# Kernel tuning notes

Hardware: AMD Instinct MI355X
Metric: run time of the kernel (lower is better)

## Reference

```python
import jax, jax.numpy as jnp
import numpy as np

N, D, F, K = 50000, 256, 256, 10


def setup_inputs() -> dict:
    key = jax.random.key(0)
    k1, k2, k3, k4, k5, k6 = jax.random.split(key, 6)
    # neighbor indices in [-1, N); -1 marks padding (masked out in forward)
    return {
        "Z1": jax.random.normal(k1, (N, D), dtype=jnp.float32),
        "Z2": jax.random.normal(k2, (N, D), dtype=jnp.float32),
        "Wr": jax.random.normal(k3, (D, F), dtype=jnp.float32),
        "Wnr": jax.random.normal(k4, (D, F), dtype=jnp.float32),
        "n1": jax.random.randint(k5, (N, K), -1, N, dtype=jnp.int64),
        "n2": jax.random.randint(k6, (N, K), -1, N, dtype=jnp.int64),
    }


def _protein(Z, nb, Wr, Wnr):
    residues_signal = Z @ Wr                      # [N, F]
    neighbors_base_signal = Z @ Wnr               # [N, F]
    mask = (nb > -1)                              # [N, K]
    # index -1 wraps to last row (as in torch), then is zeroed by the mask
    feats = neighbors_base_signal[nb] * mask[..., None].astype(Z.dtype)  # [N, K, F]
    norm = jnp.maximum(mask.sum(axis=1), 1).astype(Z.dtype)[:, None]     # [N, 1]
    neighbors_signal = feats.sum(axis=1) / norm
    return jax.nn.relu(residues_signal + neighbors_signal)


def reference(Z1, Z2, Wr, Wnr, n1, n2):
    out1 = _protein(Z1, n1, Wr, Wnr)
    out2 = _protein(Z2, n2, Wr, Wnr)
    return jnp.stack([out1, out2])  # [2, N, F]
```

## Files before the change

kernel.cpp:

```cpp
#include <hip/hip_runtime.h>
#include <hip/hip_bf16.h>
#include <hip/hip_fp8.h>

#define NNODE 50000
#define MTOT  100000
#define NF    256
#define KNB   10

typedef unsigned short u16;
typedef float f32x4 __attribute__((ext_vector_type(4)));
typedef float f32x2 __attribute__((ext_vector_type(2)));
typedef short bf16x8 __attribute__((ext_vector_type(8)));

__device__ __forceinline__ u16 f2bf(float f) {
    unsigned u = __builtin_bit_cast(unsigned, f);
    unsigned r = (u + 0x7fffu + ((u >> 16) & 1u)) >> 16;
    return (u16)r;
}
__device__ __forceinline__ unsigned char f2f8(float f) {
    return (unsigned char)__hip_fp8_e4m3(f).__x;
}
__device__ __forceinline__ float f8tof(unsigned char b) {
    __hip_fp8_e4m3 h;
    h.__x = (__hip_fp8_storage_t)b;
    return (float)h;
}
template <int WORD>
__device__ __forceinline__ f32x2 cvt2_fp8(unsigned v) {
#if __has_builtin(__builtin_amdgcn_cvt_pk_f32_fp8)
    auto c = __builtin_amdgcn_cvt_pk_f32_fp8((int)v, WORD);
    f32x2 r; r.x = c[0]; r.y = c[1];
    return r;
#else
    unsigned s = WORD ? (v >> 16) : v;
    f32x2 r;
    r.x = f8tof((unsigned char)(s & 0xff));
    r.y = f8tof((unsigned char)((s >> 8) & 0xff));
    return r;
#endif
}
template <int WORD>
__device__ __forceinline__ unsigned pk_fp8(float a, float b, unsigned old) {
#if __has_builtin(__builtin_amdgcn_cvt_pk_fp8_f32)
    return (unsigned)__builtin_amdgcn_cvt_pk_fp8_f32(a, b, (int)old, WORD);
#else
    unsigned lo = (unsigned)f2f8(a) | ((unsigned)f2f8(b) << 8);
    return WORD ? ((old & 0x0000ffffu) | (lo << 16)) : ((old & 0xffff0000u) | lo);
#endif
}
__device__ __forceinline__ void gload_lds16(const void* g, void* l) {
    __builtin_amdgcn_global_load_lds(
        (const __attribute__((address_space(1))) unsigned int*)g,
        (__attribute__((address_space(3))) unsigned int*)l, 16, 0, 0);
}

__global__ __launch_bounds__(256) void cast_all(const float* __restrict__ Z1,
                                                const float* __restrict__ Z2,
                                                const float* __restrict__ Wr,
                                                const float* __restrict__ Wnr,
                                                u16* __restrict__ Zleft,
                                                unsigned char* __restrict__ Z8,
                                                u16* __restrict__ WT,
                                                unsigned char* __restrict__ WT8) {
    int b = blockIdx.x;
    if (b < 12500) {
        unsigned id = b * 256 + threadIdx.x;
        int m = id >> 5;
        int d = (id & 31) << 3;
        const float* src = (m < NNODE) ? (Z1 + (size_t)m * 256 + d)
                                       : (Z2 + (size_t)(m - NNODE) * 256 + d);
        float4 a = *(const float4*)src;
        float4 bb = *(const float4*)(src + 4);
        uint4 o;
        o.x = (unsigned)f2bf(a.x) | ((unsigned)f2bf(a.y) << 16);
        o.y = (unsigned)f2bf(a.z) | ((unsigned)f2bf(a.w) << 16);
        o.z = (unsigned)f2bf(bb.x) | ((unsigned)f2bf(bb.y) << 16);
        o.w = (unsigned)f2bf(bb.z) | ((unsigned)f2bf(bb.w) << 16);
        *(uint4*)(Zleft + (size_t)m * 256 + d) = o;
        uint2 o8;
        o8.x = (unsigned)f2f8(a.x) | ((unsigned)f2f8(a.y) << 8) |
               ((unsigned)f2f8(a.z) << 16) | ((unsigned)f2f8(a.w) << 24);
        o8.y = (unsigned)f2f8(bb.x) | ((unsigned)f2f8(bb.y) << 8) |
               ((unsigned)f2f8(bb.z) << 16) | ((unsigned)f2f8(bb.w) << 24);
        *(uint2*)(Z8 + (size_t)m * 256 + d) = o8;
    } else if (b < 12756) {
        int id = (b - 12500) * 256 + threadIdx.x;
        int n = id >> 8, k = id & 255;
        WT[n * 256 + k] = f2bf(Wr[(size_t)k * 256 + n]);
    } else {
        int id = (b - 12756) * 256 + threadIdx.x;
        int n = id >> 8, k = id & 255;
        int kb = k ^ (((n >> 2) & 1) << 3);
        WT8[n * 256 + kb] = f2f8(Wnr[(size_t)k * 256 + n]);
    }
}

__device__ __forceinline__ void stageA(const u16* __restrict__ Zl, u16* dst,
                                       int m0, int kt, int t) {
    int row = t >> 3, gd = t & 7;
    int gs = gd ^ (row & 7);
    int grow = m0 + row;
    if (grow >= MTOT) grow = MTOT - 1;
    gload_lds16(Zl + (size_t)grow * 256 + kt + gs * 8, dst + t * 8);
}
__device__ __forceinline__ void stageBl(const u16* __restrict__ WT, u16* dst,
                                        int kt, int t) {
    #pragma unroll
    for (int rp = 0; rp < 4; ++rp) {
        int c = rp * 512 + t;
        int col = c >> 3, gd = c & 7;
        int gs = gd ^ (col & 7);
        gload_lds16(WT + (size_t)col * 256 + kt + gs * 8, dst + c * 8);
    }
}
__device__ __forceinline__ void stageBr(const unsigned char* __restrict__ WT8,
                                        unsigned char* dst, int ktr, int t) {
    #pragma unroll
    for (int rp = 0; rp < 2; ++rp) {
        int c = rp * 512 + t;
        int col = c >> 2, gd = c & 3;
        int gs = gd ^ (col & 3);
        gload_lds16(WT8 + (size_t)col * 256 + ktr + gs * 16, dst + c * 16);
    }
}

__device__ __forceinline__ void mfma_left(const u16* sAc, const u16* sBc, int lane,
                                          int wr, int wc, f32x4 (&acc)[2][4]) {
    const int hi = lane >> 4, l15 = lane & 15;
    #pragma unroll
    for (int kk = 0; kk < 64; kk += 32) {
        int g = (kk >> 3) + hi;
        bf16x8 af[2], bfr[4];
        #pragma unroll
        for (int i = 0; i < 2; ++i) {
            int row = wr * 32 + i * 16 + l15;
            af[i] = *(const bf16x8*)((const char*)sAc + row * 128 + ((g ^ (row & 7)) << 4));
        }
        #pragma unroll
        for (int j = 0; j < 4; ++j) {
            int col = wc * 64 + j * 16 + l15;
            bfr[j] = *(const bf16x8*)((const char*)sBc + col * 128 + ((g ^ (col & 7)) << 4));
        }
        #pragma unroll
        for (int i = 0; i < 2; ++i)
            #pragma unroll
            for (int j = 0; j < 4; ++j)
                acc[i][j] = __builtin_amdgcn_mfma_f32_16x16x32_bf16(af[i], bfr[j], acc[i][j], 0, 0, 0);
    }
}
__device__ __forceinline__ void mfma_right(const unsigned char* sZ, const unsigned char* sBc,
                                           int R, int lane, int wr, int wc,
                                           f32x4 (&acc)[2][4]) {
    const int hi = lane >> 4, l15 = lane & 15;
    #pragma unroll
    for (int m = 0; m < 2; ++m) {
        long long az[2], bz[4];
        #pragma unroll
        for (int i = 0; i < 2; ++i) {
            int row = wr * 32 + i * 16 + l15;
            int g8 = R * 8 + m * 4 + hi;
            az[i] = *(const long long*)(sZ + row * 256 + ((g8 ^ (row & 7)) << 3));
        }
        #pragma unroll
        for (int j = 0; j < 4; ++j) {
            int col = wc * 64 + j * 16 + l15;
            int G = 2 * m + (hi >> 1);
            int hb = ((hi & 1) ^ ((col >> 2) & 1)) << 3;
            bz[j] = *(const long long*)(sBc + col * 64 + ((G ^ (col & 3)) << 4) + hb);
        }
        #pragma unroll
        for (int i = 0; i < 2; ++i)
            #pragma unroll
            for (int j = 0; j < 4; ++j)
                acc[i][j] = __builtin_amdgcn_mfma_f32_16x16x32_fp8_fp8(az[i], bz[j], acc[i][j], 0, 0, 0);
    }
}

__device__ __forceinline__ void consume(const uint2 (&gv)[KNB], unsigned mask, int cnt,
                                        int w, int lane, int s, unsigned char* sZ) {
    f32x2 a0 = {0.f, 0.f}, a1 = {0.f, 0.f}, a2 = {0.f, 0.f}, a3 = {0.f, 0.f};
    #pragma unroll
    for (int k = 0; k < KNB; ++k) {
        float mm = (float)((mask >> k) & 1u);
        f32x2 m2 = {mm, mm};
        a0 += m2 * cvt2_fp8<0>(gv[k].x);
        a1 += m2 * cvt2_fp8<1>(gv[k].x);
        a2 += m2 * cvt2_fp8<0>(gv[k].y);
        a3 += m2 * cvt2_fp8<1>(gv[k].y);
    }
    float sc = 1.0f / (float)(cnt > 0 ? cnt : 1);
    unsigned w0 = pk_fp8<0>(a0.x * sc, a0.y * sc, 0u);
    w0 = pk_fp8<1>(a1.x * sc, a1.y * sc, w0);
    unsigned w1 = pk_fp8<0>(a2.x * sc, a2.y * sc, 0u);
    w1 = pk_fp8<1>(a3.x * sc, a3.y * sc, w1);
    int rl = w * 8 + s * 2 + (lane >> 5);
    int gp = (lane & 31) ^ (rl & 7);
    *(uint2*)(sZ + rl * 256 + (gp << 3)) = make_uint2(w0, w1);
}

template <int S>
__device__ __forceinline__ void left_step(const u16* __restrict__ Zl,
                                          const u16* __restrict__ WT,
                                          const unsigned char* __restrict__ Z8,
                                          const int* __restrict__ n1,
                                          const int* __restrict__ n2,
                                          u16* sA0, u16* sA1, u16* sBL, unsigned char* sZ,
                                          int m0, int t, int lane, int w, int wr, int wc,
                                          int2 (&icur)[5], unsigned& pmask, int& pcnt,
                                          uint2 (&gv)[KNB], f32x4 (&acc)[2][4]) {
    u16* sAcur = (S & 1) ? sA1 : sA0;
    u16* sAnxt = (S & 1) ? sA0 : sA1;
    stageBl(WT, sBL, S * 64, t);
    __builtin_amdgcn_sched_barrier(0);
    if (S < 3) stageA(Zl, sAnxt, m0, (S + 1) * 64, t);
    __builtin_amdgcn_sched_barrier(0);
    int2 inxt[5];
    if (S < 3) {
        int rl = w * 8 + (S + 1) * 2 + (lane >> 5);
        int g = m0 + rl;
        if (g >= MTOT) g = MTOT - 1;
        int p = (g >= NNODE);
        const int* nb = (p ? n2 : n1) + (size_t)(g - p * NNODE) * KNB;
        #pragma unroll
        for (int q = 0; q < 5; ++q) inxt[q] = *(const int2*)(nb + 2 * q);
    }
    __builtin_amdgcn_sched_barrier(0);
    if (S > 0) consume(gv, pmask, pcnt, w, lane, S - 1, sZ);
    __builtin_amdgcn_sched_barrier(0);
    {
        int rl = w * 8 + S * 2 + (lane >> 5);
        int g = m0 + rl;
        if (g >= MTOT) g = MTOT - 1;
        int p = (g >= NNODE);
        const unsigned char* zb = Z8 + (size_t)p * ((size_t)NNODE * 256) + ((lane & 31) << 3);
        unsigned mask = 0;
        int cnt = 0;
        #pragma unroll
        for (int k = 0; k < KNB; ++k) {
            int ix = (k & 1) ? icur[k >> 1].y : icur[k >> 1].x;
            int valid = (ix > -1) ? 1 : 0;
            mask |= (unsigned)valid << k;
            cnt += valid;
            gv[k] = *(const uint2*)(zb + (size_t)(valid ? ix : 0) * 256);
        }
        pmask = mask;
        pcnt = cnt;
    }
    if (S < 3) {
        #pragma unroll
        for (int q = 0; q < 5; ++q) icur[q] = inxt[q];
    }
    __builtin_amdgcn_sched_barrier(0);
    if (S < 3) asm volatile("s_waitcnt vmcnt(16)" ::: "memory");
    else       asm volatile("s_waitcnt vmcnt(10)" ::: "memory");
    __builtin_amdgcn_s_barrier();
    __builtin_amdgcn_s_setprio(1);
    mfma_left(sAcur, sBL, lane, wr, wc, acc);
    __builtin_amdgcn_s_setprio(0);
    __builtin_amdgcn_s_barrier();
}

__global__ __launch_bounds__(512, 4) void gemm_fused(const u16* __restrict__ Zl,
                                                     const unsigned char* __restrict__ Z8,
                                                     const u16* __restrict__ WT,
                                                     const unsigned char* __restrict__ WT8,
                                                     const int* __restrict__ n1,
                                                     const int* __restrict__ n2,
                                                     float* __restrict__ C) {
    __shared__ char smem[65536];
    u16* sA0 = (u16*)smem;
    u16* sA1 = (u16*)(smem + 8192);
    u16* sBL = (u16*)(smem + 16384);
    unsigned char* sBr0 = (unsigned char*)(smem + 16384);
    unsigned char* sBr1 = (unsigned char*)(smem + 32768);
    unsigned char* sZ = (unsigned char*)(smem + 49152);

    const int m0 = blockIdx.x * 64;
    const int t = threadIdx.x;
    const int lane = t & 63;
    const int w = t >> 6;
    const int wr = w >> 2, wc = w & 3;

    f32x4 acc[2][4] = {};
    uint2 gv[KNB];
    int2 icur[5];
    unsigned pmask = 0;
    int pcnt = 0;

    stageA(Zl, sA0, m0, 0, t);
    {
        int rl = w * 8 + (lane >> 5);
        int g = m0 + rl;
        if (g >= MTOT) g = MTOT - 1;
        int p = (g >= NNODE);
        const int* nb = (p ? n2 : n1) + (size_t)(g - p * NNODE) * KNB;
        #pragma unroll
        for (int q = 0; q < 5; ++q) icur[q] = *(const int2*)(nb + 2 * q);
    }

    left_step<0>(Zl, WT, Z8, n1, n2, sA0, sA1, sBL, sZ, m0, t, lane, w, wr, wc, icur, pmask, pcnt, gv, acc);
    left_step<1>(Zl, WT, Z8, n1, n2, sA0, sA1, sBL, sZ, m0, t, lane, w, wr, wc, icur, pmask, pcnt, gv, acc);
    left_step<2>(Zl, WT, Z8, n1, n2, sA0, sA1, sBL, sZ, m0, t, lane, w, wr, wc, icur, pmask, pcnt, gv, acc);
    left_step<3>(Zl, WT, Z8, n1, n2, sA0, sA1, sBL, sZ, m0, t, lane, w, wr, wc, icur, pmask, pcnt, gv, acc);

    consume(gv, pmask, pcnt, w, lane, 3, sZ);
    stageBr(WT8, sBr0, 0, t);
    asm volatile("s_waitcnt vmcnt(0)" ::: "memory");
    asm volatile("s_waitcnt lgkmcnt(0)" ::: "memory");
    __builtin_amdgcn_s_barrier();

#define RSTEP(R)                                                            \
    do {                                                                    \
        if ((R) < 3) {                                                      \
            stageBr(WT8, ((R) & 1) ? sBr0 : sBr1, ((R) + 1) * 64, t);       \
            asm volatile("s_waitcnt vmcnt(2)" ::: "memory");                \
        } else {                                                            \
            asm volatile("s_waitcnt vmcnt(0)" ::: "memory");                \
        }                                                                   \
        __builtin_amdgcn_s_barrier();                                       \
        __builtin_amdgcn_s_setprio(1);                                      \
        mfma_right(sZ, ((R) & 1) ? sBr1 : sBr0, (R), lane, wr, wc, acc);    \
        __builtin_amdgcn_s_setprio(0);                                      \
        if ((R) < 3) __builtin_amdgcn_s_barrier();                          \
    } while (0)

    RSTEP(0);
    RSTEP(1);
    RSTEP(2);
    RSTEP(3);
#undef RSTEP

    const int l15 = lane & 15;
    #pragma unroll
    for (int i = 0; i < 2; ++i) {
        int rbase = m0 + wr * 32 + i * 16 + ((lane >> 4) << 2);
        #pragma unroll
        for (int j = 0; j < 4; ++j) {
            int col = wc * 64 + j * 16 + l15;
            #pragma unroll
            for (int q = 0; q < 4; ++q) {
                int row = rbase + q;
                if (row < MTOT) C[(size_t)row * NF + col] = fmaxf(acc[i][j][q], 0.f);
            }
        }
    }
}

extern "C" void kernel_launch(void* const* d_in, const int* in_sizes, int n_in,
                              void* d_out, int out_size, void* d_ws, size_t ws_size,
                              hipStream_t stream) {
    const float* Z1  = (const float*)d_in[0];
    const float* Z2  = (const float*)d_in[1];
    const float* Wr  = (const float*)d_in[2];
    const float* Wnr = (const float*)d_in[3];
    const int*   n1  = (const int*)d_in[4];
    const int*   n2  = (const int*)d_in[5];
    float* out = (float*)d_out;

    u16* WT            = (u16*)d_ws;
    unsigned char* WT8 = (unsigned char*)d_ws + 131072;
    u16* Zleft         = (u16*)((unsigned char*)d_ws + 196608);
    unsigned char* Z8  = (unsigned char*)d_ws + 196608 + (size_t)MTOT * 512;

    cast_all<<<13012, 256, 0, stream>>>(Z1, Z2, Wr, Wnr, Zleft, Z8, WT, WT8);
    gemm_fused<<<1563, 512, 0, stream>>>(Zleft, Z8, WT, WT8, n1, n2, out);
}
```

Before: 110.6 us.

## Load A fragments and fp8 weights directly from global, double-buffer left weights in LDS

The left bf16 GEMM now reads its A fragments straight from global memory into registers instead of staging them through LDS. The weight tile becomes a double-buffered LDS pair, and the next tile is prefetched while MFMAs run, which removes one barrier per step. The right fp8 GEMM now reads WT8 operands directly from global (L2) instead of staging them in LDS, which drops the barriers and the XOR swizzle there. Block order is also reversed. The aim is less LDS traffic and fewer synchronisation points. The cost is uncoalesced-looking global reads in the inner loops and heavier register and cache pressure. LDS grows to 80KB, which may limit occupancy.

```diff
diff --git a/kernel.cpp b/kernel.cpp
--- a/kernel.cpp
+++ b/kernel.cpp
@@ -90,19 +90,10 @@
     } else {
         int id = (b - 12756) * 256 + threadIdx.x;
         int n = id >> 8, k = id & 255;
-        int kb = k ^ (((n >> 2) & 1) << 3);
-        WT8[n * 256 + kb] = f2f8(Wnr[(size_t)k * 256 + n]);
-    }
-}
-
-__device__ __forceinline__ void stageA(const u16* __restrict__ Zl, u16* dst,
-                                       int m0, int kt, int t) {
-    int row = t >> 3, gd = t & 7;
-    int gs = gd ^ (row & 7);
-    int grow = m0 + row;
-    if (grow >= MTOT) grow = MTOT - 1;
-    gload_lds16(Zl + (size_t)grow * 256 + kt + gs * 8, dst + t * 8);
-}
+        WT8[n * 256 + k] = f2f8(Wnr[(size_t)k * 256 + n]);
+    }
+}
+
 __device__ __forceinline__ void stageBl(const u16* __restrict__ WT, u16* dst,
                                         int kt, int t) {
     #pragma unroll
@@ -111,68 +102,6 @@
         int col = c >> 3, gd = c & 7;
         int gs = gd ^ (col & 7);
         gload_lds16(WT + (size_t)col * 256 + kt + gs * 8, dst + c * 8);
-    }
-}
-__device__ __forceinline__ void stageBr(const unsigned char* __restrict__ WT8,
-                                        unsigned char* dst, int ktr, int t) {
-    #pragma unroll
-    for (int rp = 0; rp < 2; ++rp) {
-        int c = rp * 512 + t;
-        int col = c >> 2, gd = c & 3;
-        int gs = gd ^ (col & 3);
-        gload_lds16(WT8 + (size_t)col * 256 + ktr + gs * 16, dst + c * 16);
-    }
-}
-
-__device__ __forceinline__ void mfma_left(const u16* sAc, const u16* sBc, int lane,
-                                          int wr, int wc, f32x4 (&acc)[2][4]) {
-    const int hi = lane >> 4, l15 = lane & 15;
-    #pragma unroll
-    for (int kk = 0; kk < 64; kk += 32) {
-        int g = (kk >> 3) + hi;
-        bf16x8 af[2], bfr[4];
-        #pragma unroll
-        for (int i = 0; i < 2; ++i) {
-            int row = wr * 32 + i * 16 + l15;
-            af[i] = *(const bf16x8*)((const char*)sAc + row * 128 + ((g ^ (row & 7)) << 4));
-        }
-        #pragma unroll
-        for (int j = 0; j < 4; ++j) {
-            int col = wc * 64 + j * 16 + l15;
-            bfr[j] = *(const bf16x8*)((const char*)sBc + col * 128 + ((g ^ (col & 7)) << 4));
-        }
-        #pragma unroll
-        for (int i = 0; i < 2; ++i)
-            #pragma unroll
-            for (int j = 0; j < 4; ++j)
-                acc[i][j] = __builtin_amdgcn_mfma_f32_16x16x32_bf16(af[i], bfr[j], acc[i][j], 0, 0, 0);
-    }
-}
-__device__ __forceinline__ void mfma_right(const unsigned char* sZ, const unsigned char* sBc,
-                                           int R, int lane, int wr, int wc,
-                                           f32x4 (&acc)[2][4]) {
-    const int hi = lane >> 4, l15 = lane & 15;
-    #pragma unroll
-    for (int m = 0; m < 2; ++m) {
-        long long az[2], bz[4];
-        #pragma unroll
-        for (int i = 0; i < 2; ++i) {
-            int row = wr * 32 + i * 16 + l15;
-            int g8 = R * 8 + m * 4 + hi;
-            az[i] = *(const long long*)(sZ + row * 256 + ((g8 ^ (row & 7)) << 3));
-        }
-        #pragma unroll
-        for (int j = 0; j < 4; ++j) {
-            int col = wc * 64 + j * 16 + l15;
-            int G = 2 * m + (hi >> 1);
-            int hb = ((hi & 1) ^ ((col >> 2) & 1)) << 3;
-            bz[j] = *(const long long*)(sBc + col * 64 + ((G ^ (col & 3)) << 4) + hb);
-        }
-        #pragma unroll
-        for (int i = 0; i < 2; ++i)
-            #pragma unroll
-            for (int j = 0; j < 4; ++j)
-                acc[i][j] = __builtin_amdgcn_mfma_f32_16x16x32_fp8_fp8(az[i], bz[j], acc[i][j], 0, 0, 0);
     }
 }
 
@@ -204,32 +133,28 @@
                                           const unsigned char* __restrict__ Z8,
                                           const int* __restrict__ n1,
                                           const int* __restrict__ n2,
-                                          u16* sA0, u16* sA1, u16* sBL, unsigned char* sZ,
+                                          u16* sB0, u16* sB1, unsigned char* sZ,
                                           int m0, int t, int lane, int w, int wr, int wc,
                                           int2 (&icur)[5], unsigned& pmask, int& pcnt,
                                           uint2 (&gv)[KNB], f32x4 (&acc)[2][4]) {
-    u16* sAcur = (S & 1) ? sA1 : sA0;
-    u16* sAnxt = (S & 1) ? sA0 : sA1;
-    stageBl(WT, sBL, S * 64, t);
-    __builtin_amdgcn_sched_barrier(0);
-    if (S < 3) stageA(Zl, sAnxt, m0, (S + 1) * 64, t);
-    __builtin_amdgcn_sched_barrier(0);
-    int2 inxt[5];
-    if (S < 3) {
-        int rl = w * 8 + (S + 1) * 2 + (lane >> 5);
-        int g = m0 + rl;
-        if (g >= MTOT) g = MTOT - 1;
-        int p = (g >= NNODE);
-        const int* nb = (p ? n2 : n1) + (size_t)(g - p * NNODE) * KNB;
-        #pragma unroll
-        for (int q = 0; q < 5; ++q) inxt[q] = *(const int2*)(nb + 2 * q);
+    const int hi = lane >> 4, l15 = lane & 15;
+    u16* sBcur = (S & 1) ? sB1 : sB0;
+    u16* sBnxt = (S & 1) ? sB0 : sB1;
+    bf16x8 af[2][2];
+    #pragma unroll
+    for (int k2 = 0; k2 < 2; ++k2) {
+        #pragma unroll
+        for (int i = 0; i < 2; ++i) {
+            int grow = m0 + wr * 32 + i * 16 + l15;
+            if (grow >= MTOT) grow = MTOT - 1;
+            af[k2][i] = *(const bf16x8*)(Zl + (size_t)grow * 256 + S * 64 + k2 * 32 + hi * 8);
+        }
     }
     __builtin_amdgcn_sched_barrier(0);
     if (S > 0) consume(gv, pmask, pcnt, w, lane, S - 1, sZ);
     __builtin_amdgcn_sched_barrier(0);
     {
-        int rl = w * 8 + S * 2 + (lane >> 5);
-        int g = m0 + rl;
+        int g = m0 + w * 8 + S * 2 + (lane >> 5);
         if (g >= MTOT) g = MTOT - 1;
         int p = (g >= NNODE);
         const unsigned char* zb = Z8 + (size_t)p * ((size_t)NNODE * 256) + ((lane & 31) << 3);
@@ -246,18 +171,41 @@
         pmask = mask;
         pcnt = cnt;
     }
+    __builtin_amdgcn_sched_barrier(0);
     if (S < 3) {
+        int g = m0 + w * 8 + (S + 1) * 2 + (lane >> 5);
+        if (g >= MTOT) g = MTOT - 1;
+        int p = (g >= NNODE);
+        const int* nb = (p ? n2 : n1) + (size_t)(g - p * NNODE) * KNB;
+        int2 inxt[5];
+        #pragma unroll
+        for (int q = 0; q < 5; ++q) inxt[q] = *(const int2*)(nb + 2 * q);
         #pragma unroll
         for (int q = 0; q < 5; ++q) icur[q] = inxt[q];
     }
     __builtin_amdgcn_sched_barrier(0);
-    if (S < 3) asm volatile("s_waitcnt vmcnt(16)" ::: "memory");
+    if (S < 3) asm volatile("s_waitcnt vmcnt(15)" ::: "memory");
     else       asm volatile("s_waitcnt vmcnt(10)" ::: "memory");
     __builtin_amdgcn_s_barrier();
+    __builtin_amdgcn_sched_barrier(0);
+    if (S < 3) stageBl(WT, sBnxt, (S + 1) * 64, t);
     __builtin_amdgcn_s_setprio(1);
-    mfma_left(sAcur, sBL, lane, wr, wc, acc);
+    #pragma unroll
+    for (int k2 = 0; k2 < 2; ++k2) {
+        int g = (k2 * 32 >> 3) + hi;
+        bf16x8 bfr[4];
+        #pragma unroll
+        for (int j = 0; j < 4; ++j) {
+            int col = wc * 64 + j * 16 + l15;
+            bfr[j] = *(const bf16x8*)((const char*)sBcur + col * 128 + ((g ^ (col & 7)) << 4));
+        }
+        #pragma unroll
+        for (int i = 0; i < 2; ++i)
+            #pragma unroll
+            for (int j = 0; j < 4; ++j)
+                acc[i][j] = __builtin_amdgcn_mfma_f32_16x16x32_bf16(af[k2][i], bfr[j], acc[i][j], 0, 0, 0);
+    }
     __builtin_amdgcn_s_setprio(0);
-    __builtin_amdgcn_s_barrier();
 }
 
 __global__ __launch_bounds__(512, 4) void gemm_fused(const u16* __restrict__ Zl,
@@ -267,19 +215,15 @@
                                                      const int* __restrict__ n1,
                                                      const int* __restrict__ n2,
                                                      float* __restrict__ C) {
-    __shared__ char smem[65536];
-    u16* sA0 = (u16*)smem;
-    u16* sA1 = (u16*)(smem + 8192);
-    u16* sBL = (u16*)(smem + 16384);
-    unsigned char* sBr0 = (unsigned char*)(smem + 16384);
-    unsigned char* sBr1 = (unsigned char*)(smem + 32768);
-    unsigned char* sZ = (unsigned char*)(smem + 49152);
-
-    const int m0 = blockIdx.x * 64;
+    __shared__ u16 sB0[256 * 64];
+    __shared__ u16 sB1[256 * 64];
+    __shared__ unsigned char sZ[64 * 256];
+    const int m0 = (1562 - blockIdx.x) * 64;
     const int t = threadIdx.x;
     const int lane = t & 63;
     const int w = t >> 6;
     const int wr = w >> 2, wc = w & 3;
+    const int hi = lane >> 4, l15 = lane & 15;
 
     f32x4 acc[2][4] = {};
     uint2 gv[KNB];
@@ -287,10 +231,9 @@
     unsigned pmask = 0;
     int pcnt = 0;
 
-    stageA(Zl, sA0, m0, 0, t);
+    stageBl(WT, sB0, 0, t);
     {
-        int rl = w * 8 + (lane >> 5);
-        int g = m0 + rl;
+        int g = m0 + w * 8 + (lane >> 5);
         if (g >= MTOT) g = MTOT - 1;
         int p = (g >= NNODE);
         const int* nb = (p ? n2 : n1) + (size_t)(g - p * NNODE) * KNB;
@@ -298,30 +241,38 @@
         for (int q = 0; q < 5; ++q) icur[q] = *(const int2*)(nb + 2 * q);
     }
 
-    left_step<0>(Zl, WT, Z8, n1, n2, sA0, sA1, sBL, sZ, m0, t, lane, w, wr, wc, icur, pmask, pcnt, gv, acc);
-    left_step<1>(Zl, WT, Z8, n1, n2, sA0, sA1, sBL, sZ, m0, t, lane, w, wr, wc, icur, pmask, pcnt, gv, acc);
-    left_step<2>(Zl, WT, Z8, n1, n2, sA0, sA1, sBL, sZ, m0, t, lane, w, wr, wc, icur, pmask, pcnt, gv, acc);
-    left_step<3>(Zl, WT, Z8, n1, n2, sA0, sA1, sBL, sZ, m0, t, lane, w, wr, wc, icur, pmask, pcnt, gv, acc);
+    left_step<0>(Zl, WT, Z8, n1, n2, sB0, sB1, sZ, m0, t, lane, w, wr, wc, icur, pmask, pcnt, gv, acc);
+    left_step<1>(Zl, WT, Z8, n1, n2, sB0, sB1, sZ, m0, t, lane, w, wr, wc, icur, pmask, pcnt, gv, acc);
+    left_step<2>(Zl, WT, Z8, n1, n2, sB0, sB1, sZ, m0, t, lane, w, wr, wc, icur, pmask, pcnt, gv, acc);
+    left_step<3>(Zl, WT, Z8, n1, n2, sB0, sB1, sZ, m0, t, lane, w, wr, wc, icur, pmask, pcnt, gv, acc);
 
     consume(gv, pmask, pcnt, w, lane, 3, sZ);
-    stageBr(WT8, sBr0, 0, t);
-    asm volatile("s_waitcnt vmcnt(0)" ::: "memory");
-    asm volatile("s_waitcnt lgkmcnt(0)" ::: "memory");
-    __builtin_amdgcn_s_barrier();
-
-#define RSTEP(R)                                                            \
-    do {                                                                    \
-        if ((R) < 3) {                                                      \
-            stageBr(WT8, ((R) & 1) ? sBr0 : sBr1, ((R) + 1) * 64, t);       \
-            asm volatile("s_waitcnt vmcnt(2)" ::: "memory");                \
-        } else {                                                            \
-            asm volatile("s_waitcnt vmcnt(0)" ::: "memory");                \
-        }                                                                   \
-        __builtin_amdgcn_s_barrier();                                       \
-        __builtin_amdgcn_s_setprio(1);                                      \
-        mfma_right(sZ, ((R) & 1) ? sBr1 : sBr0, (R), lane, wr, wc, acc);    \
-        __builtin_amdgcn_s_setprio(0);                                      \
-        if ((R) < 3) __builtin_amdgcn_s_barrier();                          \
+    __syncthreads();
+
+#define RSTEP(R)                                                              \
+    do {                                                                      \
+        __builtin_amdgcn_s_setprio(1);                                        \
+        _Pragma("unroll")                                                     \
+        for (int m = 0; m < 2; ++m) {                                         \
+            long long az[2], bz[4];                                           \
+            _Pragma("unroll")                                                 \
+            for (int i = 0; i < 2; ++i) {                                     \
+                int row = wr * 32 + i * 16 + l15;                             \
+                int g8 = (R) * 8 + m * 4 + hi;                                \
+                az[i] = *(const long long*)(sZ + row * 256 + ((g8 ^ (row & 7)) << 3)); \
+            }                                                                 \
+            _Pragma("unroll")                                                 \
+            for (int j = 0; j < 4; ++j) {                                     \
+                int col = wc * 64 + j * 16 + l15;                             \
+                bz[j] = *(const long long*)(WT8 + (size_t)col * 256 + (R) * 64 + m * 32 + hi * 8); \
+            }                                                                 \
+            _Pragma("unroll")                                                 \
+            for (int i = 0; i < 2; ++i)                                       \
+                _Pragma("unroll")                                             \
+                for (int j = 0; j < 4; ++j)                                   \
+                    acc[i][j] = __builtin_amdgcn_mfma_f32_16x16x32_fp8_fp8(az[i], bz[j], acc[i][j], 0, 0, 0); \
+        }                                                                     \
+        __builtin_amdgcn_s_setprio(0);                                        \
     } while (0)
 
     RSTEP(0);
@@ -330,10 +281,9 @@
     RSTEP(3);
 #undef RSTEP
 
-    const int l15 = lane & 15;
     #pragma unroll
     for (int i = 0; i < 2; ++i) {
-        int rbase = m0 + wr * 32 + i * 16 + ((lane >> 4) << 2);
+        int rbase = m0 + wr * 32 + i * 16 + (hi << 2);
         #pragma unroll
         for (int j = 0; j < 4; ++j) {
             int col = wc * 64 + j * 16 + l15;
```

New measurement: 192.2 us. 73.8% more time.

## Restructure fused GEMM pipeline with triple-buffered half-K B tiles

Applied to the files above, without the earlier changes.

Splits each 64-wide K step of the bf16 left GEMM into two 32-wide halves and rotates the B weight tiles through a three-slot LDS ring shared with the fp8 right-GEMM tiles. The goal is to prefetch further ahead and remove one barrier per step. The right-GEMM prologue is overlapped with the last left steps, and blocks are launched in reverse order. Manual vmcnt counts are tuned by hand, so a miscount could cause a race or an over-wait.

```diff
diff --git a/kernel.cpp b/kernel.cpp
--- a/kernel.cpp
+++ b/kernel.cpp
@@ -103,13 +103,13 @@
     if (grow >= MTOT) grow = MTOT - 1;
     gload_lds16(Zl + (size_t)grow * 256 + kt + gs * 8, dst + t * 8);
 }
-__device__ __forceinline__ void stageBl(const u16* __restrict__ WT, u16* dst,
+__device__ __forceinline__ void stageBh(const u16* __restrict__ WT, u16* dst,
                                         int kt, int t) {
     #pragma unroll
-    for (int rp = 0; rp < 4; ++rp) {
+    for (int rp = 0; rp < 2; ++rp) {
         int c = rp * 512 + t;
-        int col = c >> 3, gd = c & 7;
-        int gs = gd ^ (col & 7);
+        int col = c >> 2, gd = c & 3;
+        int gs = gd ^ (col & 3);
         gload_lds16(WT + (size_t)col * 256 + kt + gs * 8, dst + c * 8);
     }
 }
@@ -121,58 +121,6 @@
         int col = c >> 2, gd = c & 3;
         int gs = gd ^ (col & 3);
         gload_lds16(WT8 + (size_t)col * 256 + ktr + gs * 16, dst + c * 16);
-    }
-}
-
-__device__ __forceinline__ void mfma_left(const u16* sAc, const u16* sBc, int lane,
-                                          int wr, int wc, f32x4 (&acc)[2][4]) {
-    const int hi = lane >> 4, l15 = lane & 15;
-    #pragma unroll
-    for (int kk = 0; kk < 64; kk += 32) {
-        int g = (kk >> 3) + hi;
-        bf16x8 af[2], bfr[4];
-        #pragma unroll
-        for (int i = 0; i < 2; ++i) {
-            int row = wr * 32 + i * 16 + l15;
-            af[i] = *(const bf16x8*)((const char*)sAc + row * 128 + ((g ^ (row & 7)) << 4));
-        }
-        #pragma unroll
-        for (int j = 0; j < 4; ++j) {
-            int col = wc * 64 + j * 16 + l15;
-            bfr[j] = *(const bf16x8*)((const char*)sBc + col * 128 + ((g ^ (col & 7)) << 4));
-        }
-        #pragma unroll
-        for (int i = 0; i < 2; ++i)
-            #pragma unroll
-            for (int j = 0; j < 4; ++j)
-                acc[i][j] = __builtin_amdgcn_mfma_f32_16x16x32_bf16(af[i], bfr[j], acc[i][j], 0, 0, 0);
-    }
-}
-__device__ __forceinline__ void mfma_right(const unsigned char* sZ, const unsigned char* sBc,
-                                           int R, int lane, int wr, int wc,
-                                           f32x4 (&acc)[2][4]) {
-    const int hi = lane >> 4, l15 = lane & 15;
-    #pragma unroll
-    for (int m = 0; m < 2; ++m) {
-        long long az[2], bz[4];
-        #pragma unroll
-        for (int i = 0; i < 2; ++i) {
-            int row = wr * 32 + i * 16 + l15;
-            int g8 = R * 8 + m * 4 + hi;
-            az[i] = *(const long long*)(sZ + row * 256 + ((g8 ^ (row & 7)) << 3));
-        }
-        #pragma unroll
-        for (int j = 0; j < 4; ++j) {
-            int col = wc * 64 + j * 16 + l15;
-            int G = 2 * m + (hi >> 1);
-            int hb = ((hi & 1) ^ ((col >> 2) & 1)) << 3;
-            bz[j] = *(const long long*)(sBc + col * 64 + ((G ^ (col & 3)) << 4) + hb);
-        }
-        #pragma unroll
-        for (int i = 0; i < 2; ++i)
-            #pragma unroll
-            for (int j = 0; j < 4; ++j)
-                acc[i][j] = __builtin_amdgcn_mfma_f32_16x16x32_fp8_fp8(az[i], bz[j], acc[i][j], 0, 0, 0);
     }
 }
 
@@ -198,66 +146,52 @@
     *(uint2*)(sZ + rl * 256 + (gp << 3)) = make_uint2(w0, w1);
 }
 
-template <int S>
-__device__ __forceinline__ void left_step(const u16* __restrict__ Zl,
-                                          const u16* __restrict__ WT,
-                                          const unsigned char* __restrict__ Z8,
-                                          const int* __restrict__ n1,
-                                          const int* __restrict__ n2,
-                                          u16* sA0, u16* sA1, u16* sBL, unsigned char* sZ,
-                                          int m0, int t, int lane, int w, int wr, int wc,
-                                          int2 (&icur)[5], unsigned& pmask, int& pcnt,
-                                          uint2 (&gv)[KNB], f32x4 (&acc)[2][4]) {
-    u16* sAcur = (S & 1) ? sA1 : sA0;
-    u16* sAnxt = (S & 1) ? sA0 : sA1;
-    stageBl(WT, sBL, S * 64, t);
-    __builtin_amdgcn_sched_barrier(0);
-    if (S < 3) stageA(Zl, sAnxt, m0, (S + 1) * 64, t);
-    __builtin_amdgcn_sched_barrier(0);
-    int2 inxt[5];
-    if (S < 3) {
-        int rl = w * 8 + (S + 1) * 2 + (lane >> 5);
-        int g = m0 + rl;
-        if (g >= MTOT) g = MTOT - 1;
-        int p = (g >= NNODE);
-        const int* nb = (p ? n2 : n1) + (size_t)(g - p * NNODE) * KNB;
-        #pragma unroll
-        for (int q = 0; q < 5; ++q) inxt[q] = *(const int2*)(nb + 2 * q);
-    }
-    __builtin_amdgcn_sched_barrier(0);
-    if (S > 0) consume(gv, pmask, pcnt, w, lane, S - 1, sZ);
-    __builtin_amdgcn_sched_barrier(0);
-    {
-        int rl = w * 8 + S * 2 + (lane >> 5);
-        int g = m0 + rl;
-        if (g >= MTOT) g = MTOT - 1;
-        int p = (g >= NNODE);
-        const unsigned char* zb = Z8 + (size_t)p * ((size_t)NNODE * 256) + ((lane & 31) << 3);
-        unsigned mask = 0;
-        int cnt = 0;
-        #pragma unroll
-        for (int k = 0; k < KNB; ++k) {
-            int ix = (k & 1) ? icur[k >> 1].y : icur[k >> 1].x;
-            int valid = (ix > -1) ? 1 : 0;
-            mask |= (unsigned)valid << k;
-            cnt += valid;
-            gv[k] = *(const uint2*)(zb + (size_t)(valid ? ix : 0) * 256);
+__device__ __forceinline__ void mfma_halfL(const u16* sAc, const u16* sBc, int k2,
+                                           int lane, int wr, int wc, f32x4 (&acc)[2][4]) {
+    const int hi = lane >> 4, l15 = lane & 15;
+    bf16x8 af[2], bfr[4];
+    #pragma unroll
+    for (int i = 0; i < 2; ++i) {
+        int row = wr * 32 + i * 16 + l15;
+        af[i] = *(const bf16x8*)((const char*)sAc + row * 128 + (((k2 * 4 + hi) ^ (row & 7)) << 4));
+    }
+    #pragma unroll
+    for (int j = 0; j < 4; ++j) {
+        int col = wc * 64 + j * 16 + l15;
+        bfr[j] = *(const bf16x8*)((const char*)sBc + col * 64 + ((hi ^ (col & 3)) << 4));
+    }
+    #pragma unroll
+    for (int i = 0; i < 2; ++i)
+        #pragma unroll
+        for (int j = 0; j < 4; ++j)
+            acc[i][j] = __builtin_amdgcn_mfma_f32_16x16x32_bf16(af[i], bfr[j], acc[i][j], 0, 0, 0);
+}
+__device__ __forceinline__ void mfma_right(const unsigned char* sZ, const unsigned char* sBc,
+                                           int R, int lane, int wr, int wc,
+                                           f32x4 (&acc)[2][4]) {
+    const int hi = lane >> 4, l15 = lane & 15;
+    #pragma unroll
+    for (int m = 0; m < 2; ++m) {
+        long long az[2], bz[4];
+        #pragma unroll
+        for (int i = 0; i < 2; ++i) {
+            int row = wr * 32 + i * 16 + l15;
+            int g8 = R * 8 + m * 4 + hi;
+            az[i] = *(const long long*)(sZ + row * 256 + ((g8 ^ (row & 7)) << 3));
         }
-        pmask = mask;
-        pcnt = cnt;
-    }
-    if (S < 3) {
-        #pragma unroll
-        for (int q = 0; q < 5; ++q) icur[q] = inxt[q];
-    }
-    __builtin_amdgcn_sched_barrier(0);
-    if (S < 3) asm volatile("s_waitcnt vmcnt(16)" ::: "memory");
-    else       asm volatile("s_waitcnt vmcnt(10)" ::: "memory");
-    __builtin_amdgcn_s_barrier();
-    __builtin_amdgcn_s_setprio(1);
-    mfma_left(sAcur, sBL, lane, wr, wc, acc);
-    __builtin_amdgcn_s_setprio(0);
-    __builtin_amdgcn_s_barrier();
+        #pragma unroll
+        for (int j = 0; j < 4; ++j) {
+            int col = wc * 64 + j * 16 + l15;
+            int G = 2 * m + (hi >> 1);
+            int hb = ((hi & 1) ^ ((col >> 2) & 1)) << 3;
+            bz[j] = *(const long long*)(sBc + col * 64 + ((G ^ (col & 3)) << 4) + hb);
+        }
+        #pragma unroll
+        for (int i = 0; i < 2; ++i)
+            #pragma unroll
+            for (int j = 0; j < 4; ++j)
+                acc[i][j] = __builtin_amdgcn_mfma_f32_16x16x32_fp8_fp8(az[i], bz[j], acc[i][j], 0, 0, 0);
+    }
 }
 
 __global__ __launch_bounds__(512, 4) void gemm_fused(const u16* __restrict__ Zl,
@@ -267,19 +201,15 @@
                                                      const int* __restrict__ n1,
                                                      const int* __restrict__ n2,
                                                      float* __restrict__ C) {
-    __shared__ char smem[65536];
-    u16* sA0 = (u16*)smem;
-    u16* sA1 = (u16*)(smem + 8192);
-    u16* sBL = (u16*)(smem + 16384);
-    unsigned char* sBr0 = (unsigned char*)(smem + 16384);
-    unsigned char* sBr1 = (unsigned char*)(smem + 32768);
-    unsigned char* sZ = (unsigned char*)(smem + 49152);
-
-    const int m0 = blockIdx.x * 64;
+    __shared__ u16 sA[2][64 * 64];
+    __shared__ u16 sB[3][256 * 32];
+    __shared__ unsigned char sZ[64 * 256];
+    const int m0 = (1562 - blockIdx.x) * 64;
     const int t = threadIdx.x;
     const int lane = t & 63;
     const int w = t >> 6;
     const int wr = w >> 2, wc = w & 3;
+    const int hi = lane >> 4, l15 = lane & 15;
 
     f32x4 acc[2][4] = {};
     uint2 gv[KNB];
@@ -287,41 +217,99 @@
     unsigned pmask = 0;
     int pcnt = 0;
 
-    stageA(Zl, sA0, m0, 0, t);
     {
-        int rl = w * 8 + (lane >> 5);
-        int g = m0 + rl;
+        int g = m0 + w * 8 + (lane >> 5);
         if (g >= MTOT) g = MTOT - 1;
         int p = (g >= NNODE);
         const int* nb = (p ? n2 : n1) + (size_t)(g - p * NNODE) * KNB;
         #pragma unroll
         for (int q = 0; q < 5; ++q) icur[q] = *(const int2*)(nb + 2 * q);
     }
-
-    left_step<0>(Zl, WT, Z8, n1, n2, sA0, sA1, sBL, sZ, m0, t, lane, w, wr, wc, icur, pmask, pcnt, gv, acc);
-    left_step<1>(Zl, WT, Z8, n1, n2, sA0, sA1, sBL, sZ, m0, t, lane, w, wr, wc, icur, pmask, pcnt, gv, acc);
-    left_step<2>(Zl, WT, Z8, n1, n2, sA0, sA1, sBL, sZ, m0, t, lane, w, wr, wc, icur, pmask, pcnt, gv, acc);
-    left_step<3>(Zl, WT, Z8, n1, n2, sA0, sA1, sBL, sZ, m0, t, lane, w, wr, wc, icur, pmask, pcnt, gv, acc);
+    stageA(Zl, &sA[0][0], m0, 0, t);
+    stageBh(WT, &sB[0][0], 0, t);
+    stageBh(WT, &sB[1][0], 32, t);
+
+#define LH0(S)                                                                 \
+    do {                                                                       \
+         \
+        if ((S) == 0) asm volatile("s_waitcnt vmcnt(2)" ::: "memory");         \
+        else          asm volatile("s_waitcnt vmcnt(17)" ::: "memory");        \
+        __builtin_amdgcn_s_barrier();                                          \
+        if ((S) < 3) stageBh(WT, &sB[(2 * (S) + 2) % 3][0], (2 * (S) + 2) * 32, t); \
+        else         stageBr(WT8, (unsigned char*)&sB[2][0], 0, t);            \
+        if ((S) < 3) stageA(Zl, &sA[((S) + 1) & 1][0], m0, ((S) + 1) * 64, t); \
+        __builtin_amdgcn_sched_barrier(0);                                     \
+        if ((S) > 0) consume(gv, pmask, pcnt, w, lane, (S) - 1, sZ);           \
+        __builtin_amdgcn_sched_barrier(0);                                     \
+        {                                                      \
+            int g = m0 + w * 8 + (S) * 2 + (lane >> 5);                        \
+            if (g >= MTOT) g = MTOT - 1;                                       \
+            int p = (g >= NNODE);                                              \
+            const unsigned char* zb = Z8 + (size_t)p * ((size_t)NNODE * 256) + ((lane & 31) << 3); \
+            unsigned mask = 0;                                                 \
+            int cnt = 0;                                                       \
+            _Pragma("unroll")                                                  \
+            for (int k = 0; k < KNB; ++k) {                                    \
+                int ix = (k & 1) ? icur[k >> 1].y : icur[k >> 1].x;            \
+                int valid = (ix > -1) ? 1 : 0;                                 \
+                mask |= (unsigned)valid << k;                                  \
+                cnt += valid;                                                  \
+                gv[k] = *(const uint2*)(zb + (size_t)(valid ? ix : 0) * 256);  \
+            }                                                                  \
+            pmask = mask;                                                      \
+            pcnt = cnt;                                                        \
+        }                                                                      \
+        if ((S) < 3) {                                           \
+            int g = m0 + w * 8 + ((S) + 1) * 2 + (lane >> 5);                  \
+            if (g >= MTOT) g = MTOT - 1;                                       \
+            int p = (g >= NNODE);                                              \
+            const int* nb = (p ? n2 : n1) + (size_t)(g - p * NNODE) * KNB;     \
+            _Pragma("unroll")                                                  \
+            for (int q = 0; q < 5; ++q) icur[q] = *(const int2*)(nb + 2 * q);  \
+        }                                                                      \
+        __builtin_amdgcn_sched_barrier(0);                                     \
+        __builtin_amdgcn_s_setprio(1);                                         \
+        mfma_halfL(&sA[(S) & 1][0], &sB[(2 * (S)) % 3][0], 0, lane, wr, wc, acc); \
+        __builtin_amdgcn_s_setprio(0);                                         \
+    } while (0)
+
+#define LH1(S)                                                                 \
+    do {                                                                       \
+               \
+        if ((S) < 3) asm volatile("s_waitcnt vmcnt(18)" ::: "memory");         \
+        else         asm volatile("s_waitcnt vmcnt(12)" ::: "memory");         \
+        __builtin_amdgcn_s_barrier();                                          \
+        if ((S) < 3) stageBh(WT, &sB[(2 * (S) + 3) % 3][0], (2 * (S) + 3) * 32, t); \
+        else         stageBr(WT8, (unsigned char*)&sB[0][0], 64, t);           \
+        __builtin_amdgcn_sched_barrier(0);                                     \
+        __builtin_amdgcn_s_setprio(1);                                         \
+        mfma_halfL(&sA[(S) & 1][0], &sB[(2 * (S) + 1) % 3][0], 1, lane, wr, wc, acc); \
+        __builtin_amdgcn_s_setprio(0);                                         \
+    } while (0)
+
+    LH0(0); LH1(0);
+    LH0(1); LH1(1);
+    LH0(2); LH1(2);
+    LH0(3); LH1(3);
+#undef LH0
+#undef LH1
 
     consume(gv, pmask, pcnt, w, lane, 3, sZ);
-    stageBr(WT8, sBr0, 0, t);
-    asm volatile("s_waitcnt vmcnt(0)" ::: "memory");
     asm volatile("s_waitcnt lgkmcnt(0)" ::: "memory");
+    asm volatile("s_waitcnt vmcnt(2)" ::: "memory");
     __builtin_amdgcn_s_barrier();
 
-#define RSTEP(R)                                                            \
-    do {                                                                    \
-        if ((R) < 3) {                                                      \
-            stageBr(WT8, ((R) & 1) ? sBr0 : sBr1, ((R) + 1) * 64, t);       \
-            asm volatile("s_waitcnt vmcnt(2)" ::: "memory");                \
-        } else {                                                            \
-            asm volatile("s_waitcnt vmcnt(0)" ::: "memory");                \
-        }                                                                   \
-        __builtin_amdgcn_s_barrier();                                       \
-        __builtin_amdgcn_s_setprio(1);                                      \
-        mfma_right(sZ, ((R) & 1) ? sBr1 : sBr0, (R), lane, wr, wc, acc);    \
-        __builtin_amdgcn_s_setprio(0);                                      \
-        if ((R) < 3) __builtin_amdgcn_s_barrier();                          \
+#define RSTEP(R)                                                               \
+    do {                                                                       \
+        if ((R) > 0) {                                                         \
+            if ((R) < 3) asm volatile("s_waitcnt vmcnt(2)" ::: "memory");      \
+            else         asm volatile("s_waitcnt vmcnt(0)" ::: "memory");      \
+            __builtin_amdgcn_s_barrier();                                      \
+        }                                                                      \
+        if ((R) < 2) stageBr(WT8, (unsigned char*)&sB[((R) + 10) % 3][0], ((R) + 2) * 64, t); \
+        __builtin_amdgcn_s_setprio(1);                                         \
+        mfma_right(sZ, (const unsigned char*)&sB[((R) + 8) % 3][0], (R), lane, wr, wc, acc); \
+        __builtin_amdgcn_s_setprio(0);                                         \
     } while (0)
 
     RSTEP(0);
@@ -330,10 +318,9 @@
     RSTEP(3);
 #undef RSTEP
 
-    const int l15 = lane & 15;
     #pragma unroll
     for (int i = 0; i < 2; ++i) {
-        int rbase = m0 + wr * 32 + i * 16 + ((lane >> 4) << 2);
+        int rbase = m0 + wr * 32 + i * 16 + (hi << 2);
         #pragma unroll
         for (int j = 0; j < 4; ++j) {
             int col = wc * 64 + j * 16 + l15;
```

After: 121.1 us. +9.5%, slower.
